# Kernel tuning notes

Measured on AMD Instinct MI355X. Metric: run time of the kernel, lower is better.

Reference implementation:

```python
import jax, jax.numpy as jnp
import numpy as np

D_MODEL = 768; N_LAYER = 4; D_STATE = 64; D_CONV = 4; EXPAND = 2; HEADDIM = 64
D_INNER = EXPAND * D_MODEL          # 1536
NHEADS = D_INNER // HEADDIM         # 24
CONV_DIM = D_INNER + 2 * D_STATE    # 1664
D_IN_PROJ = 2 * D_INNER + 2 * D_STATE + NHEADS  # 3224
VOCAB = 50257; EPS = 1e-5


def _ln(x, w, b):
    m = x.mean(-1, keepdims=True)
    v = ((x - m) ** 2).mean(-1, keepdims=True)
    return (x - m) * jax.lax.rsqrt(v + EPS) * w + b


def _silu(x):
    return x * jax.nn.sigmoid(x)


def _mamba2(x, W_in, conv_w, conv_b, dt_bias, A_log, Dp, rms_w, W_out):
    # x: [B, L, d_model]
    Bsz, L, _ = x.shape
    zxbcdt = x @ W_in.T                                   # [B,L,D_IN_PROJ]
    z = zxbcdt[..., :D_INNER]
    xBC = zxbcdt[..., D_INNER:D_INNER + CONV_DIM]
    dt = zxbcdt[..., D_INNER + CONV_DIM:]                 # [B,L,H]
    # causal depthwise conv over time
    xc = jnp.transpose(xBC, (0, 2, 1))                    # [B,C,L]
    xc = jax.lax.conv_general_dilated(
        xc, conv_w[:, None, :], (1,), [(D_CONV - 1, 0)],
        dimension_numbers=('NCH', 'OIH', 'NCH'), feature_group_count=CONV_DIM)
    xBC = _silu(jnp.transpose(xc, (0, 2, 1)) + conv_b)
    xh = xBC[..., :D_INNER].reshape(Bsz, L, NHEADS, HEADDIM)
    Bc = xBC[..., D_INNER:D_INNER + D_STATE]              # [B,L,N]
    Cc = xBC[..., D_INNER + D_STATE:]                     # [B,L,N]
    dt = jax.nn.softplus(dt + dt_bias)                    # [B,L,H]
    dA = jnp.exp(dt * (-jnp.exp(A_log)))                  # [B,L,H]

    def step(h, inp):
        dA_t, dt_t, x_t, B_t, C_t = inp
        h = dA_t[:, :, None, None] * h + (dt_t[:, :, None] * x_t)[..., None] * B_t[:, None, None, :]
        return h, jnp.einsum('bhpn,bn->bhp', h, C_t)

    tm = lambda a: jnp.moveaxis(a, 1, 0)  # time-major
    h0 = jnp.zeros((Bsz, NHEADS, HEADDIM, D_STATE), x.dtype)
    _, y = jax.lax.scan(step, h0, (tm(dA), tm(dt), tm(xh), tm(Bc), tm(Cc)))
    y = jnp.moveaxis(y, 0, 1) + Dp[:, None] * xh          # [B,L,H,P]
    y = y.reshape(Bsz, L, D_INNER) * _silu(z)             # gate
    y = y * jax.lax.rsqrt((y * y).mean(-1, keepdims=True) + EPS) * rms_w
    return y @ W_out.T


def setup_inputs() -> dict:
    key = jax.random.key(0)
    ks = jax.random.split(key, 16)
    B, L = 1, 1024
    idx = jax.random.randint(ks[0], (B, L), 0, VOCAB)
    targets = jax.random.randint(ks[1], (B, L), 0, VOCAB)
    s = 0.02
    emb = jax.random.normal(ks[2], (VOCAB, D_MODEL), jnp.float32) * s
    ln_w = jnp.ones((N_LAYER, D_MODEL)); ln_b = jnp.zeros((N_LAYER, D_MODEL))
    W_in = jax.random.normal(ks[3], (N_LAYER, D_IN_PROJ, D_MODEL), jnp.float32) * s
    conv_w = jax.random.normal(ks[4], (N_LAYER, CONV_DIM, D_CONV), jnp.float32) * 0.1
    conv_b = jnp.zeros((N_LAYER, CONV_DIM))
    dt_bias = jnp.log(jnp.expm1(jax.random.uniform(ks[5], (N_LAYER, NHEADS), minval=0.001, maxval=0.1)))
    A_log = jnp.log(jax.random.uniform(ks[6], (N_LAYER, NHEADS), minval=1.0, maxval=16.0))
    Dp = jnp.ones((N_LAYER, NHEADS))
    rms_w = jnp.ones((N_LAYER, D_INNER))
    W_out = jax.random.normal(ks[7], (N_LAYER, D_MODEL, D_INNER), jnp.float32) * s
    lnf_w = jnp.ones((D_MODEL,)); lnf_b = jnp.zeros((D_MODEL,))
    return {"idx": idx, "targets": targets, "emb": emb, "ln_w": ln_w, "ln_b": ln_b,
            "W_in": W_in, "conv_w": conv_w, "conv_b": conv_b, "dt_bias": dt_bias,
            "A_log": A_log, "Dp": Dp, "rms_w": rms_w, "W_out": W_out,
            "lnf_w": lnf_w, "lnf_b": lnf_b}


def reference(idx, targets, emb, ln_w, ln_b, W_in, conv_w, conv_b, dt_bias,
              A_log, Dp, rms_w, W_out, lnf_w, lnf_b):
    x = emb[idx]                                          # [B,L,D]
    for i in range(N_LAYER):
        x = x + _mamba2(_ln(x, ln_w[i], ln_b[i]), W_in[i], conv_w[i], conv_b[i],
                        dt_bias[i], A_log[i], Dp[i], rms_w[i], W_out[i])
    x = _ln(x, lnf_w, lnf_b)
    logits = x @ emb.T                                    # tied head
    logp = jax.nn.log_softmax(logits, axis=-1)
    loss = -jnp.take_along_axis(logp, targets[..., None], axis=-1).mean()
    return logits, loss
```

## Files before the change

kernel.cpp:

```cpp
#include <hip/hip_runtime.h>
#include <hip/hip_bf16.h>
#include <math.h>

#define SL     1024
#define DMODEL 768
#define NLAYER 4
#define NSTATE 64
#define HEADDIM 64
#define DINNER 1536
#define NHEADS 24
#define CONVDIM 1664
#define DINPROJ 3224
#define VOCABN 50257

typedef __attribute__((ext_vector_type(8))) short short8;
typedef __attribute__((ext_vector_type(4))) short short4v;
typedef __attribute__((ext_vector_type(4))) float f32x4;

__device__ __forceinline__ short f2bf(float f) {
    unsigned int u = __builtin_bit_cast(unsigned int, f);
    u += 0x7fffu + ((u >> 16) & 1u);
    return (short)(u >> 16);
}

#define AS1 __attribute__((address_space(1)))
#define AS3 __attribute__((address_space(3)))
__device__ __forceinline__ void gl2lds16(const void* g, void* l) {
    __builtin_amdgcn_global_load_lds((const AS1 unsigned int*)g,
                                     (AS3 unsigned int*)(unsigned int)(uintptr_t)l,
                                     16, 0, 0);
}

template <int CTRL>
__device__ __forceinline__ float dppadd(float x) {
    int v = __builtin_amdgcn_update_dpp(0, __builtin_bit_cast(int, x), CTRL, 0xf, 0xf, true);
    return x + __builtin_bit_cast(float, v);
}

__global__ void cvt_k(const float* __restrict__ s, short* __restrict__ d, int n) {
    int i = (blockIdx.x * 256 + threadIdx.x) * 4;
    if (i >= n) return;
    float4 v = *(const float4*)(s + i);
    short4v o;
    o.x = f2bf(v.x); o.y = f2bf(v.y); o.z = f2bf(v.z); o.w = f2bf(v.w);
    *(short4v*)(d + i) = o;
}

__global__ void embed_k(const int* __restrict__ idx, const float* __restrict__ emb,
                        float* __restrict__ x) {
    int d = blockIdx.x * 256 + threadIdx.x;
    int t = blockIdx.y;
    x[t * DMODEL + d] = emb[(size_t)idx[t] * DMODEL + d];
}

__global__ void ln_k(const float* __restrict__ x, const float* __restrict__ w,
                     const float* __restrict__ b, short* __restrict__ out) {
    int row = blockIdx.x, t = threadIdx.x;
    const float* xr = x + row * DMODEL;
    float v0 = xr[t], v1 = xr[t + 256], v2 = xr[t + 512];
    float s = v0 + v1 + v2;
    float q = v0 * v0 + v1 * v1 + v2 * v2;
    __shared__ float sa[4], sb[4];
    for (int off = 32; off; off >>= 1) { s += __shfl_down(s, off); q += __shfl_down(q, off); }
    if (!(t & 63)) { sa[t >> 6] = s; sb[t >> 6] = q; }
    __syncthreads();
    s = sa[0] + sa[1] + sa[2] + sa[3];
    q = sb[0] + sb[1] + sb[2] + sb[3];
    float mean = s * (1.f / DMODEL);
    float var  = q * (1.f / DMODEL) - mean * mean;
    float rs = rsqrtf(var + 1e-5f);
    out[row * DMODEL + t      ] = f2bf((v0 - mean) * rs * w[t      ] + b[t      ]);
    out[row * DMODEL + t + 256] = f2bf((v1 - mean) * rs * w[t + 256] + b[t + 256]);
    out[row * DMODEL + t + 512] = f2bf((v2 - mean) * rs * w[t + 512] + b[t + 512]);
}

__global__ __launch_bounds__(512) void gemm_bb_k(const short* __restrict__ A,
                                                 const short* __restrict__ B,
                                                 float* __restrict__ C,
                                                 float2* __restrict__ P,
                                                 int N, int K, int addflag) {
    __shared__ __align__(16) short As[2][16384];
    __shared__ __align__(16) short Bs[2][16384];
    const int t = threadIdx.x;
    const int lane = t & 63, wv = t >> 6;

    const int nwg = gridDim.x;
    int bid = blockIdx.x;
    int qq = nwg >> 3, rr = nwg & 7;
    int xcd = bid & 7, ii = bid >> 3;
    int v = (xcd < rr ? xcd * (qq + 1) : rr * (qq + 1) + (xcd - rr) * qq) + ii;
    const int m0 = (v & 3) * 256;
    const int n0 = (v >> 2) * 256;

    const int wm = (wv >> 2) * 128, wn = (wv & 3) * 64;
    const int q4 = lane >> 4, l16 = lane & 15;
    const int abase = (wm >> 7) * 8192;
    const int bbase = (wn >> 7) * 8192 + (wn & 64) * 8;

    f32x4 zero4 = {0.f, 0.f, 0.f, 0.f};
    f32x4 acc[8][4];
#pragma unroll
    for (int i = 0; i < 8; i++)
#pragma unroll
        for (int j = 0; j < 4; j++) acc[i][j] = zero4;

    auto stageA = [&](int buf, int half, int k0) {
#pragma unroll
        for (int i = 0; i < 2; i++) {
            int g = i * 512 + t;
            int q = g >> 7, rh = g & 127;
            gl2lds16(A + (size_t)(m0 + half * 128 + rh) * K + k0 + q * 8,
                     &As[buf][half * 8192 + g * 8]);
        }
    };
    auto stageB = [&](int buf, int half, int k0) {
#pragma unroll
        for (int i = 0; i < 2; i++) {
            int g = i * 512 + t;
            int q = g >> 7, rh = g & 127;
            int gr = n0 + half * 128 + rh; if (gr > N - 1) gr = N - 1;
            gl2lds16(B + (size_t)gr * K + k0 + q * 8,
                     &Bs[buf][half * 8192 + g * 8]);
        }
    };

    const int NT = K >> 6;
    stageA(0, 0, 0); stageA(0, 1, 0); stageB(0, 0, 0); stageB(0, 1, 0);

    for (int tt = 0; tt < NT; tt++) {
        const int cur = tt & 1;
        const bool pf = (tt + 1 < NT);
        const int k1 = (tt + 1) << 6;
        const short* Ac = &As[cur][abase];
        const short* Bc = &Bs[cur][bbase];

        asm volatile("s_waitcnt vmcnt(0)" ::: "memory");
        __builtin_amdgcn_s_barrier();

        short8 bfk[4];
        {
            short8 af[4];
#pragma unroll
            for (int nt = 0; nt < 4; nt++)
                bfk[nt] = *(const short8*)(Bc + q4 * 1024 + (nt * 16 + l16) * 8);
#pragma unroll
            for (int mt = 0; mt < 4; mt++)
                af[mt] = *(const short8*)(Ac + q4 * 1024 + (mt * 16 + l16) * 8);
            if (pf) { stageA(cur ^ 1, 0, k1); stageA(cur ^ 1, 1, k1); }
            __builtin_amdgcn_s_barrier();
            __builtin_amdgcn_s_setprio(1);
#pragma unroll
            for (int mt = 0; mt < 4; mt++)
#pragma unroll
                for (int nt = 0; nt < 4; nt++)
                    acc[mt][nt] = __builtin_amdgcn_mfma_f32_16x16x32_bf16(af[mt], bfk[nt], acc[mt][nt], 0, 0, 0);
            __builtin_amdgcn_s_setprio(0);
            __builtin_amdgcn_s_barrier();
        }
        {
            short8 af[4];
#pragma unroll
            for (int mt = 0; mt < 4; mt++)
                af[mt] = *(const short8*)(Ac + q4 * 1024 + ((mt + 4) * 16 + l16) * 8);
            if (pf) { stageB(cur ^ 1, 0, k1); stageB(cur ^ 1, 1, k1); }
            __builtin_amdgcn_s_barrier();
            __builtin_amdgcn_s_setprio(1);
#pragma unroll
            for (int mt = 0; mt < 4; mt++)
#pragma unroll
                for (int nt = 0; nt < 4; nt++)
                    acc[mt + 4][nt] = __builtin_amdgcn_mfma_f32_16x16x32_bf16(af[mt], bfk[nt], acc[mt + 4][nt], 0, 0, 0);
            __builtin_amdgcn_s_setprio(0);
            __builtin_amdgcn_s_barrier();
        }
        {
            short8 af[4];
#pragma unroll
            for (int nt = 0; nt < 4; nt++)
                bfk[nt] = *(const short8*)(Bc + (4 + q4) * 1024 + (nt * 16 + l16) * 8);
#pragma unroll
            for (int mt = 0; mt < 4; mt++)
                af[mt] = *(const short8*)(Ac + (4 + q4) * 1024 + (mt * 16 + l16) * 8);
            __builtin_amdgcn_s_barrier();
            __builtin_amdgcn_s_setprio(1);
#pragma unroll
            for (int mt = 0; mt < 4; mt++)
#pragma unroll
                for (int nt = 0; nt < 4; nt++)
                    acc[mt][nt] = __builtin_amdgcn_mfma_f32_16x16x32_bf16(af[mt], bfk[nt], acc[mt][nt], 0, 0, 0);
            __builtin_amdgcn_s_setprio(0);
            __builtin_amdgcn_s_barrier();
        }
        {
            short8 af[4];
#pragma unroll
            for (int mt = 0; mt < 4; mt++)
                af[mt] = *(const short8*)(Ac + (4 + q4) * 1024 + ((mt + 4) * 16 + l16) * 8);
            __builtin_amdgcn_s_barrier();
            __builtin_amdgcn_s_setprio(1);
#pragma unroll
            for (int mt = 0; mt < 4; mt++)
#pragma unroll
                for (int nt = 0; nt < 4; nt++)
                    acc[mt + 4][nt] = __builtin_amdgcn_mfma_f32_16x16x32_bf16(af[mt], bfk[nt], acc[mt + 4][nt], 0, 0, 0);
            __builtin_amdgcn_s_setprio(0);
            __builtin_amdgcn_s_barrier();
        }
    }

#pragma unroll
    for (int mt = 0; mt < 8; mt++) {
        int row = m0 + wm + mt * 16 + q4 * 4;
#pragma unroll
        for (int nt = 0; nt < 4; nt++) {
            int col = n0 + wn + nt * 16 + l16;
            if (col < N) {
#pragma unroll
                for (int r = 0; r < 4; r++) {
                    size_t o = (size_t)(row + r) * N + col;
                    float val = acc[mt][nt][r];
                    if (addflag) C[o] += val; else C[o] = val;
                }
            }
        }
    }

    float2* lds_ms = (float2*)&As[0][0];
    const int nw = wv & 3;
#pragma unroll
    for (int mt = 0; mt < 8; mt++) {
#pragma unroll
        for (int r = 0; r < 4; r++) {
            float m = -3.0e38f;
#pragma unroll
            for (int nt = 0; nt < 4; nt++) {
                int col = n0 + wn + nt * 16 + l16;
                if (col < N) m = fmaxf(m, acc[mt][nt][r]);
            }
#pragma unroll
            for (int off = 1; off < 16; off <<= 1)
                m = fmaxf(m, __shfl_xor(m, off));
            float s = 0.f;
#pragma unroll
            for (int nt = 0; nt < 4; nt++) {
                int col = n0 + wn + nt * 16 + l16;
                if (col < N) s += __expf(acc[mt][nt][r] - m);
            }
#pragma unroll
            for (int off = 1; off < 16; off <<= 1)
                s += __shfl_xor(s, off);
            if (l16 == 0)
                lds_ms[(wm + mt * 16 + q4 * 4 + r) * 5 + nw] = make_float2(m, s);
        }
    }
    __syncthreads();
    if (t < 256) {
        float m = -3.0e38f, s = 0.f;
#pragma unroll
        for (int w = 0; w < 4; w++) {
            float2 p = lds_ms[t * 5 + w];
            float nm = fmaxf(m, p.x);
            s = s * __expf(m - nm) + p.y * __expf(p.x - nm);
            m = nm;
        }
        P[(size_t)(v >> 2) * 1024 + (m0 + t)] = make_float2(m, s);
    }
}

__global__ __launch_bounds__(256) void gemm64_k(const short* __restrict__ A,
                                                const short* __restrict__ B,
                                                float* __restrict__ C,
                                                int N, int K, int addflag, int nMB) {
    __shared__ __align__(16) short As[2][4096];
    __shared__ __align__(16) short Bs[2][4096];
    const int t = threadIdx.x;
    const int lane = t & 63, wv = t >> 6;

    const int nwg = gridDim.x;
    int bid = blockIdx.x;
    int qq = nwg >> 3, rr = nwg & 7;
    int xcd = bid & 7, ii = bid >> 3;
    int v = (xcd < rr ? xcd * (qq + 1) : rr * (qq + 1) + (xcd - rr) * qq) + ii;
    const int m0 = (v % nMB) * 64, n0 = (v / nMB) * 64;

    const int wm = (wv >> 1) * 32, wn = (wv & 1) * 32;
    const int q4 = lane >> 4, l16 = lane & 15;

    f32x4 zero4 = {0.f, 0.f, 0.f, 0.f};
    f32x4 acc[2][2];
#pragma unroll
    for (int i = 0; i < 2; i++)
#pragma unroll
        for (int j = 0; j < 2; j++) acc[i][j] = zero4;

    auto stage = [&](int buf, int k0) {
#pragma unroll
        for (int i = 0; i < 2; i++) {
            int g = i * 256 + t;
            int q = g >> 6, r = g & 63;
            gl2lds16(A + (size_t)(m0 + r) * K + k0 + q * 8, &As[buf][g * 8]);
        }
#pragma unroll
        for (int i = 0; i < 2; i++) {
            int g = i * 256 + t;
            int q = g >> 6, r = g & 63;
            int gr = n0 + r; if (gr > N - 1) gr = N - 1;
            gl2lds16(B + (size_t)gr * K + k0 + q * 8, &Bs[buf][g * 8]);
        }
    };

    const int NT = K >> 6;
    stage(0, 0);
    for (int tt = 0; tt < NT; tt++) {
        const int cur = tt & 1;
        if (tt + 1 < NT) {
            stage(cur ^ 1, (tt + 1) << 6);
            asm volatile("s_waitcnt vmcnt(4)" ::: "memory");
        } else {
            asm volatile("s_waitcnt vmcnt(0)" ::: "memory");
        }
        __builtin_amdgcn_s_barrier();

        short8 af[2][2], bf[2][2];
#pragma unroll
        for (int kk = 0; kk < 2; kk++) {
#pragma unroll
            for (int mt = 0; mt < 2; mt++)
                af[kk][mt] = *(const short8*)(&As[cur][(kk * 4 + q4) * 512 + (wm + mt * 16 + l16) * 8]);
#pragma unroll
            for (int nt = 0; nt < 2; nt++)
                bf[kk][nt] = *(const short8*)(&Bs[cur][(kk * 4 + q4) * 512 + (wn + nt * 16 + l16) * 8]);
        }
        asm volatile("s_waitcnt lgkmcnt(0)" ::: "memory");
        __builtin_amdgcn_s_barrier();

#pragma unroll
        for (int kk = 0; kk < 2; kk++)
#pragma unroll
            for (int mt = 0; mt < 2; mt++)
#pragma unroll
                for (int nt = 0; nt < 2; nt++)
                    acc[mt][nt] = __builtin_amdgcn_mfma_f32_16x16x32_bf16(af[kk][mt], bf[kk][nt], acc[mt][nt], 0, 0, 0);
    }

#pragma unroll
    for (int mt = 0; mt < 2; mt++) {
        int row = m0 + wm + mt * 16 + (lane >> 4) * 4;
#pragma unroll
        for (int nt = 0; nt < 2; nt++) {
            int col = n0 + wn + nt * 16 + l16;
            if (col < N) {
#pragma unroll
                for (int r = 0; r < 4; r++) {
                    size_t o = (size_t)(row + r) * N + col;
                    float val = acc[mt][nt][r];
                    if (addflag) C[o] += val; else C[o] = val;
                }
            }
        }
    }
}

#define LDSK 56
__global__ __launch_bounds__(256) void gemm_bt_k(const short* __restrict__ A,
                                                 const float* __restrict__ B,
                                                 float* __restrict__ C,
                                                 int N, int K, int addflag) {
    __shared__ __align__(16) short As[128 * LDSK];
    __shared__ __align__(16) short Bs[128 * LDSK];
    const int t = threadIdx.x;
    const int lane = t & 63, wv = t >> 6;
    const int m0 = blockIdx.x * 128, n0 = blockIdx.y * 128;
    const int wm = (wv >> 1) * 64, wn = (wv & 1) * 64;
    f32x4 zero4 = {0.f, 0.f, 0.f, 0.f};
    f32x4 acc[4][4];
#pragma unroll
    for (int i = 0; i < 4; i++)
#pragma unroll
        for (int j = 0; j < 4; j++) acc[i][j] = zero4;
    for (int k0 = 0; k0 < K; k0 += 32) {
        uint4  av[2];
        float4 bv[4];
#pragma unroll
        for (int i = 0; i < 2; i++) {
            int c = i * 256 + t, row = c >> 2, kc = c & 3;
            av[i] = *(const uint4*)(A + (size_t)(m0 + row) * K + k0 + kc * 8);
        }
#pragma unroll
        for (int i = 0; i < 4; i++) {
            int c = i * 256 + t, row = c >> 3, kc = c & 7;
            int gr = n0 + row; if (gr > N - 1) gr = N - 1;
            bv[i] = *(const float4*)(B + (size_t)gr * K + k0 + kc * 4);
        }
        __syncthreads();
#pragma unroll
        for (int i = 0; i < 2; i++) {
            int c = i * 256 + t, row = c >> 2, kc = c & 3;
            *(uint4*)(As + row * LDSK + kc * 8) = av[i];
        }
#pragma unroll
        for (int i = 0; i < 4; i++) {
            int c = i * 256 + t, row = c >> 3, kc = c & 7;
            short4v sv;
            sv.x = f2bf(bv[i].x); sv.y = f2bf(bv[i].y);
            sv.z = f2bf(bv[i].z); sv.w = f2bf(bv[i].w);
            *(short4v*)(Bs + row * LDSK + kc * 4) = sv;
        }
        __syncthreads();
        short8 af[4], bf[4];
#pragma unroll
        for (int mt = 0; mt < 4; mt++)
            af[mt] = *(const short8*)(As + (wm + mt * 16 + (lane & 15)) * LDSK + (lane >> 4) * 8);
#pragma unroll
        for (int nt = 0; nt < 4; nt++)
            bf[nt] = *(const short8*)(Bs + (wn + nt * 16 + (lane & 15)) * LDSK + (lane >> 4) * 8);
#pragma unroll
        for (int mt = 0; mt < 4; mt++)
#pragma unroll
            for (int nt = 0; nt < 4; nt++)
                acc[mt][nt] = __builtin_amdgcn_mfma_f32_16x16x32_bf16(af[mt], bf[nt], acc[mt][nt], 0, 0, 0);
    }
#pragma unroll
    for (int mt = 0; mt < 4; mt++) {
        int row = m0 + wm + mt * 16 + (lane >> 4) * 4;
#pragma unroll
        for (int nt = 0; nt < 4; nt++) {
            int col = n0 + wn + nt * 16 + (lane & 15);
            if (col < N) {
#pragma unroll
                for (int r = 0; r < 4; r++) {
                    size_t o = (size_t)(row + r) * N + col;
                    float val = acc[mt][nt][r];
                    if (addflag) C[o] += val; else C[o] = val;
                }
            }
        }
    }
}

__global__ void convdt_k(const float* __restrict__ zx, const float* __restrict__ cw,
                         const float* __restrict__ cb, const float* __restrict__ dt_bias,
                         const float* __restrict__ A_log, float* __restrict__ xbc,
                         float* __restrict__ dts, float* __restrict__ dAv) {
    int c = blockIdx.x * 256 + threadIdx.x;
    int t = blockIdx.y;
    if (c < CONVDIM) {
        float acc = cb[c];
#pragma unroll
        for (int j = 0; j < 4; j++) {
            int ts = t - 3 + j;
            if (ts >= 0) acc += cw[c * 4 + j] * zx[(size_t)ts * DINPROJ + DINNER + c];
        }
        xbc[(size_t)t * CONVDIM + c] = acc / (1.f + __expf(-acc));
    } else if (c < CONVDIM + NHEADS) {
        int h = c - CONVDIM;
        float d = zx[(size_t)t * DINPROJ + 3200 + h] + dt_bias[h];
        float sp = (d > 20.f) ? d : log1pf(__expf(d));
        dts[t * NHEADS + h] = sp;
        dAv[t * NHEADS + h] = __expf(-__expf(A_log[h]) * sp);
    }
}

__global__ __launch_bounds__(128) void scan_k(const float* __restrict__ xbc,
                                              const float* __restrict__ dts,
                                              const float* __restrict__ dAv,
                                              float* __restrict__ yraw) {
    __shared__ __align__(16) float BCs[64][128];
    __shared__ __align__(16) float xs[64][8];
    __shared__ float dash[64];
    int h = blockIdx.x >> 3;
    int pbase = (blockIdx.x & 7) * 8;
    int t = threadIdx.x, lane = t & 63, wv = t >> 6;
    int pl = wv * 4 + (lane >> 4);
    int n4 = lane & 15;
    float s0 = 0.f, s1 = 0.f, s2 = 0.f, s3 = 0.f;

    for (int tc = 0; tc < 16; tc++) {
        __syncthreads();
#pragma unroll 4
        for (int it = 0; it < 16; it++) {
            int idx = it * 128 + t;
            int trow = idx >> 5, c4 = idx & 31;
            *(float4*)&BCs[trow][c4 * 4] =
                *(const float4*)(xbc + (size_t)(tc * 64 + trow) * CONVDIM + DINNER + c4 * 4);
        }
        {
            int trow = t >> 1, hf = t & 1;
            float dtv = dts[(tc * 64 + trow) * NHEADS + h];
            float4 xv = *(const float4*)(xbc + (size_t)(tc * 64 + trow) * CONVDIM
                                         + h * HEADDIM + pbase + hf * 4);
            xv.x *= dtv; xv.y *= dtv; xv.z *= dtv; xv.w *= dtv;
            *(float4*)&xs[trow][hf * 4] = xv;
        }
        if (t < 64) dash[t] = dAv[(tc * 64 + t) * NHEADS + h];
        __syncthreads();

#pragma unroll 4
        for (int tt = 0; tt < 64; tt++) {
            float4 B4 = *(const float4*)&BCs[tt][n4 * 4];
            float4 C4 = *(const float4*)&BCs[tt][64 + n4 * 4];
            float dtx = xs[tt][pl];
            float da = dash[tt];
            s0 = fmaf(da, s0, dtx * B4.x);
            s1 = fmaf(da, s1, dtx * B4.y);
            s2 = fmaf(da, s2, dtx * B4.z);
            s3 = fmaf(da, s3, dtx * B4.w);
            float part = s0 * C4.x;
            part = fmaf(s1, C4.y, part);
            part = fmaf(s2, C4.z, part);
            part = fmaf(s3, C4.w, part);
            part = dppadd<0xB1>(part);
            part = dppadd<0x4E>(part);
            part = dppadd<0x114>(part);
            part = dppadd<0x118>(part);
            if (n4 == 0)
                yraw[(size_t)(tc * 64 + tt) * DINNER + h * HEADDIM + pbase + pl] = part;
        }
    }
}

__global__ void rms_k(const float* __restrict__ yraw, const float* __restrict__ zx,
                      const float* __restrict__ xbc, const float* __restrict__ Dp,
                      const float* __restrict__ rw, short* __restrict__ yn) {
    int row = blockIdx.x, t = threadIdx.x;
    float v[6];
    float q = 0.f;
#pragma unroll
    for (int j = 0; j < 6; j++) {
        int i = t + j * 256;
        float z  = zx[(size_t)row * DINPROJ + i];
        float xh = xbc[(size_t)row * CONVDIM + i];
        float y  = yraw[(size_t)row * DINNER + i] + Dp[i >> 6] * xh;
        float val = y * (z / (1.f + __expf(-z)));
        v[j] = val;
        q += val * val;
    }
    __shared__ float sb[4];
    for (int off = 32; off; off >>= 1) q += __shfl_down(q, off);
    if (!(t & 63)) sb[t >> 6] = q;
    __syncthreads();
    q = sb[0] + sb[1] + sb[2] + sb[3];
    float rs = rsqrtf(q * (1.f / DINNER) + 1e-5f);
#pragma unroll
    for (int j = 0; j < 6; j++) {
        int i = t + j * 256;
        yn[(size_t)row * DINNER + i] = f2bf(v[j] * rs * rw[i]);
    }
}

__global__ void loss_row_k(const float* __restrict__ logits, const int* __restrict__ tg,
                           float* __restrict__ lossp) {
    int r = blockIdx.x, t = threadIdx.x;
    const float* lr = logits + (size_t)r * VOCABN;
    float m = -3.0e38f, s = 0.f;
    for (int j = t; j < VOCABN; j += 256) {
        float v = lr[j];
        if (v > m) { s = s * __expf(m - v) + 1.f; m = v; }
        else s += __expf(v - m);
    }
    for (int off = 32; off; off >>= 1) {
        float mo = __shfl_down(m, off), so = __shfl_down(s, off);
        float nm = fmaxf(m, mo);
        s = s * __expf(m - nm) + so * __expf(mo - nm);
        m = nm;
    }
    __shared__ float sm[4], ss[4];
    if (!(t & 63)) { sm[t >> 6] = m; ss[t >> 6] = s; }
    __syncthreads();
    if (t == 0) {
        m = sm[0]; s = ss[0];
        for (int w = 1; w < 4; w++) {
            float nm = fmaxf(m, sm[w]);
            s = s * __expf(m - nm) + ss[w] * __expf(sm[w] - nm);
            m = nm;
        }
        lossp[r] = (m + logf(s)) - lr[tg[r]];
    }
}

__global__ void loss_fin2_k(const float2* __restrict__ P, const float* __restrict__ logits,
                            const int* __restrict__ tg, float* __restrict__ lossp) {
    int r = blockIdx.x * 256 + threadIdx.x;
    float m = -3.0e38f, s = 0.f;
    for (int p = 0; p < 197; p++) {
        float2 q = P[(size_t)p * 1024 + r];
        float nm = fmaxf(m, q.x);
        s = s * __expf(m - nm) + q.y * __expf(q.x - nm);
        m = nm;
    }
    lossp[r] = (m + logf(s)) - logits[(size_t)r * VOCABN + tg[r]];
}

__global__ void loss_fin_k(const float* __restrict__ lossp, float* __restrict__ out) {
    int t = threadIdx.x;
    float s = lossp[t] + lossp[t + 256] + lossp[t + 512] + lossp[t + 768];
    for (int off = 32; off; off >>= 1) s += __shfl_down(s, off);
    __shared__ float sb[4];
    if (!(t & 63)) sb[t >> 6] = s;
    __syncthreads();
    if (t == 0) out[(size_t)SL * VOCABN] = (sb[0] + sb[1] + sb[2] + sb[3]) * (1.f / SL);
}

extern "C" void kernel_launch(void* const* d_in, const int* in_sizes, int n_in,
                              void* d_out, int out_size, void* d_ws, size_t ws_size,
                              hipStream_t stream) {
    const int*   idx     = (const int*)d_in[0];
    const int*   targets = (const int*)d_in[1];
    const float* emb     = (const float*)d_in[2];
    const float* ln_w    = (const float*)d_in[3];
    const float* ln_b    = (const float*)d_in[4];
    const float* W_in    = (const float*)d_in[5];
    const float* conv_w  = (const float*)d_in[6];
    const float* conv_b  = (const float*)d_in[7];
    const float* dt_bias = (const float*)d_in[8];
    const float* A_log   = (const float*)d_in[9];
    const float* Dp      = (const float*)d_in[10];
    const float* rms_w   = (const float*)d_in[11];
    const float* W_out   = (const float*)d_in[12];
    const float* lnf_w   = (const float*)d_in[13];
    const float* lnf_b   = (const float*)d_in[14];

    char* ws = (char*)d_ws;
    float* x     = (float*)(ws + 0);
    short* xn    = (short*)(ws + 3145728);
    float* zx    = (float*)(ws + 4718592);
    float* xbc   = (float*)(ws + 17924096);
    float* dts   = (float*)(ws + 24739840);
    float* dAv   = (float*)(ws + 24838144);
    float* yraw  = (float*)(ws + 24936448);
    short* yn    = (short*)(ws + 31227904);
    float* lossp = (float*)(ws + 34373632);
    short* wInb  = (short*)(ws + 34377728);
    short* wOutb = (short*)(ws + 54183936);
    short* embb  = (short*)(ws + 63621120);
    float2* pms  = (float2*)(ws + 4718592);
    float* logits = (float*)d_out;

    const bool big = ws_size >= 140815872ull;

    if (big) {
        int nWin  = NLAYER * DINPROJ * DMODEL;
        int nWout = NLAYER * DMODEL * DINNER;
        int nEmb  = VOCABN * DMODEL;
        cvt_k<<<(nWin / 4 + 255) / 256, 256, 0, stream>>>(W_in, wInb, nWin);
        cvt_k<<<(nWout / 4 + 255) / 256, 256, 0, stream>>>(W_out, wOutb, nWout);
        cvt_k<<<(nEmb / 4 + 255) / 256, 256, 0, stream>>>(emb, embb, nEmb);
    }

    embed_k<<<dim3(3, SL), 256, 0, stream>>>(idx, emb, x);
    for (int l = 0; l < NLAYER; l++) {
        ln_k<<<SL, 256, 0, stream>>>(x, ln_w + l * DMODEL, ln_b + l * DMODEL, xn);
        if (big)
            gemm64_k<<<816, 256, 0, stream>>>(xn, wInb + (size_t)l * DINPROJ * DMODEL,
                                              zx, DINPROJ, DMODEL, 0, 16);
        else
            gemm_bt_k<<<dim3(8, 26), 256, 0, stream>>>(xn, W_in + (size_t)l * DINPROJ * DMODEL,
                                                       zx, DINPROJ, DMODEL, 0);
        convdt_k<<<dim3(7, SL), 256, 0, stream>>>(zx, conv_w + l * CONVDIM * 4,
                                                  conv_b + l * CONVDIM,
                                                  dt_bias + l * NHEADS, A_log + l * NHEADS,
                                                  xbc, dts, dAv);
        scan_k<<<192, 128, 0, stream>>>(xbc, dts, dAv, yraw);
        rms_k<<<SL, 256, 0, stream>>>(yraw, zx, xbc, Dp + l * NHEADS, rms_w + l * DINNER, yn);
        if (big)
            gemm64_k<<<192, 256, 0, stream>>>(yn, wOutb + (size_t)l * DMODEL * DINNER,
                                              x, DMODEL, DINNER, 1, 16);
        else
            gemm_bt_k<<<dim3(8, 6), 256, 0, stream>>>(yn, W_out + (size_t)l * DMODEL * DINNER,
                                                      x, DMODEL, DINNER, 1);
    }
    ln_k<<<SL, 256, 0, stream>>>(x, lnf_w, lnf_b, xn);
    if (big) {
        gemm_bb_k<<<4 * 197, 512, 0, stream>>>(xn, embb, logits, pms, VOCABN, DMODEL, 0);
        loss_fin2_k<<<4, 256, 0, stream>>>(pms, logits, targets, lossp);
    } else {
        gemm_bt_k<<<dim3(8, 393), 256, 0, stream>>>(xn, emb, logits, VOCABN, DMODEL, 0);
        loss_row_k<<<SL, 256, 0, stream>>>(logits, targets, lossp);
    }
    loss_fin_k<<<1, 256, 0, stream>>>(lossp, logits);
}
```

Before: 1.129 ms.

## Split GEMM LDS staging by K-half and use partial vmcnt waits

Shared-memory tiles are re-laid out by K-half (each half covers all 256 rows for 32 k-values) instead of by row-half. Prefetches for the next tile are spread across all four compute phases, and the full vmcnt(0) wait at the top of each iteration becomes partial vmcnt(4) waits after each half. Each half of the next buffer can then be consumed while the other half's loads are still in flight, hiding more global-load latency behind MFMA work. This relies on the vmcnt accounting being correct and adds more interleaving of loads with compute.

```diff
diff --git a/kernel.cpp b/kernel.cpp
--- a/kernel.cpp
+++ b/kernel.cpp
@@ -94,8 +94,6 @@
 
     const int wm = (wv >> 2) * 128, wn = (wv & 3) * 64;
     const int q4 = lane >> 4, l16 = lane & 15;
-    const int abase = (wm >> 7) * 8192;
-    const int bbase = (wn >> 7) * 8192 + (wn & 64) * 8;
 
     f32x4 zero4 = {0.f, 0.f, 0.f, 0.f};
     f32x4 acc[8][4];
@@ -104,49 +102,48 @@
 #pragma unroll
         for (int j = 0; j < 4; j++) acc[i][j] = zero4;
 
-    auto stageA = [&](int buf, int half, int k0) {
+    auto stageA = [&](int buf, int kh, int k0) {
 #pragma unroll
         for (int i = 0; i < 2; i++) {
             int g = i * 512 + t;
-            int q = g >> 7, rh = g & 127;
-            gl2lds16(A + (size_t)(m0 + half * 128 + rh) * K + k0 + q * 8,
-                     &As[buf][half * 8192 + g * 8]);
+            int q = g >> 8, r = g & 255;
+            gl2lds16(A + (size_t)(m0 + r) * K + k0 + kh * 32 + q * 8,
+                     &As[buf][kh * 8192 + g * 8]);
         }
     };
-    auto stageB = [&](int buf, int half, int k0) {
+    auto stageB = [&](int buf, int kh, int k0) {
 #pragma unroll
         for (int i = 0; i < 2; i++) {
             int g = i * 512 + t;
-            int q = g >> 7, rh = g & 127;
-            int gr = n0 + half * 128 + rh; if (gr > N - 1) gr = N - 1;
-            gl2lds16(B + (size_t)gr * K + k0 + q * 8,
-                     &Bs[buf][half * 8192 + g * 8]);
+            int q = g >> 8, r = g & 255;
+            int gr = n0 + r; if (gr > N - 1) gr = N - 1;
+            gl2lds16(B + (size_t)gr * K + k0 + kh * 32 + q * 8,
+                     &Bs[buf][kh * 8192 + g * 8]);
         }
     };
 
     const int NT = K >> 6;
-    stageA(0, 0, 0); stageA(0, 1, 0); stageB(0, 0, 0); stageB(0, 1, 0);
+    stageA(0, 0, 0); stageB(0, 0, 0); stageA(0, 1, 0); stageB(0, 1, 0);
+    asm volatile("s_waitcnt vmcnt(4)" ::: "memory");
+    __builtin_amdgcn_s_barrier();
 
     for (int tt = 0; tt < NT; tt++) {
         const int cur = tt & 1;
         const bool pf = (tt + 1 < NT);
         const int k1 = (tt + 1) << 6;
-        const short* Ac = &As[cur][abase];
-        const short* Bc = &Bs[cur][bbase];
-
-        asm volatile("s_waitcnt vmcnt(0)" ::: "memory");
-        __builtin_amdgcn_s_barrier();
+        const short* Ac = &As[cur][0];
+        const short* Bc = &Bs[cur][0];
 
         short8 bfk[4];
         {
             short8 af[4];
 #pragma unroll
             for (int nt = 0; nt < 4; nt++)
-                bfk[nt] = *(const short8*)(Bc + q4 * 1024 + (nt * 16 + l16) * 8);
-#pragma unroll
-            for (int mt = 0; mt < 4; mt++)
-                af[mt] = *(const short8*)(Ac + q4 * 1024 + (mt * 16 + l16) * 8);
-            if (pf) { stageA(cur ^ 1, 0, k1); stageA(cur ^ 1, 1, k1); }
+                bfk[nt] = *(const short8*)(Bc + q4 * 2048 + (wn + nt * 16 + l16) * 8);
+#pragma unroll
+            for (int mt = 0; mt < 4; mt++)
+                af[mt] = *(const short8*)(Ac + q4 * 2048 + (wm + mt * 16 + l16) * 8);
+            if (pf) stageA(cur ^ 1, 0, k1);
             __builtin_amdgcn_s_barrier();
             __builtin_amdgcn_s_setprio(1);
 #pragma unroll
@@ -161,8 +158,8 @@
             short8 af[4];
 #pragma unroll
             for (int mt = 0; mt < 4; mt++)
-                af[mt] = *(const short8*)(Ac + q4 * 1024 + ((mt + 4) * 16 + l16) * 8);
-            if (pf) { stageB(cur ^ 1, 0, k1); stageB(cur ^ 1, 1, k1); }
+                af[mt] = *(const short8*)(Ac + q4 * 2048 + (wm + (mt + 4) * 16 + l16) * 8);
+            if (pf) stageB(cur ^ 1, 0, k1);
             __builtin_amdgcn_s_barrier();
             __builtin_amdgcn_s_setprio(1);
 #pragma unroll
@@ -171,16 +168,19 @@
                 for (int nt = 0; nt < 4; nt++)
                     acc[mt + 4][nt] = __builtin_amdgcn_mfma_f32_16x16x32_bf16(af[mt], bfk[nt], acc[mt + 4][nt], 0, 0, 0);
             __builtin_amdgcn_s_setprio(0);
+            if (pf) asm volatile("s_waitcnt vmcnt(4)" ::: "memory");
+            else    asm volatile("s_waitcnt vmcnt(0)" ::: "memory");
             __builtin_amdgcn_s_barrier();
         }
         {
             short8 af[4];
 #pragma unroll
             for (int nt = 0; nt < 4; nt++)
-                bfk[nt] = *(const short8*)(Bc + (4 + q4) * 1024 + (nt * 16 + l16) * 8);
-#pragma unroll
-            for (int mt = 0; mt < 4; mt++)
-                af[mt] = *(const short8*)(Ac + (4 + q4) * 1024 + (mt * 16 + l16) * 8);
+                bfk[nt] = *(const short8*)(Bc + 8192 + q4 * 2048 + (wn + nt * 16 + l16) * 8);
+#pragma unroll
+            for (int mt = 0; mt < 4; mt++)
+                af[mt] = *(const short8*)(Ac + 8192 + q4 * 2048 + (wm + mt * 16 + l16) * 8);
+            if (pf) stageA(cur ^ 1, 1, k1);
             __builtin_amdgcn_s_barrier();
             __builtin_amdgcn_s_setprio(1);
 #pragma unroll
@@ -195,7 +195,8 @@
             short8 af[4];
 #pragma unroll
             for (int mt = 0; mt < 4; mt++)
-                af[mt] = *(const short8*)(Ac + (4 + q4) * 1024 + ((mt + 4) * 16 + l16) * 8);
+                af[mt] = *(const short8*)(Ac + 8192 + q4 * 2048 + (wm + (mt + 4) * 16 + l16) * 8);
+            if (pf) stageB(cur ^ 1, 1, k1);
             __builtin_amdgcn_s_barrier();
             __builtin_amdgcn_s_setprio(1);
 #pragma unroll
@@ -204,6 +205,8 @@
                 for (int nt = 0; nt < 4; nt++)
                     acc[mt + 4][nt] = __builtin_amdgcn_mfma_f32_16x16x32_bf16(af[mt], bfk[nt], acc[mt + 4][nt], 0, 0, 0);
             __builtin_amdgcn_s_setprio(0);
+            if (pf) asm volatile("s_waitcnt vmcnt(4)" ::: "memory");
+            else    asm volatile("s_waitcnt vmcnt(0)" ::: "memory");
             __builtin_amdgcn_s_barrier();
         }
     }
```

New measurement: 1.123 ms. No clear change (-0.5%).
